# Kernel tuning notes

Measured on AMD Instinct MI355X. Metric: run time of the kernel, lower is better.

The kernel has to match this reference:

```python
import jax, jax.numpy as jnp
import numpy as np

# GraphConvolutionSparse forward:
#   x = sparse_dropout(X)            (dropout=0.0 -> identity, kept faithful)
#   h = X @ W                        (sparse-dense matmul via segment_sum)
#   h = A @ h                        (sparse-dense matmul via segment_sum)
#   out = relu(h)

DROPOUT = 0.0  # layer default; keep_prob = 1 - dropout

def setup_inputs() -> dict:
    key = jax.random.key(0)
    k1, k2, k3, k4, k5, k6, k7 = jax.random.split(key, 7)
    N = 100000       # nodes
    D_IN = 512       # input feature dim
    D_OUT = 128      # output feature dim
    NNZ_X = 800000   # nonzeros in sparse feature matrix
    N_E = 1600000    # adjacency nonzeros (edges)
    x_vals = jax.random.normal(k1, (NNZ_X,), dtype=jnp.float32)
    x_rows = jax.random.randint(k2, (NNZ_X,), 0, N, dtype=jnp.int32)
    x_cols = jax.random.randint(k3, (NNZ_X,), 0, D_IN, dtype=jnp.int32)
    adj_vals = jax.random.uniform(k4, (N_E,), dtype=jnp.float32)
    adj_rows = jax.random.randint(k5, (N_E,), 0, N, dtype=jnp.int32)
    adj_cols = jax.random.randint(k6, (N_E,), 0, N, dtype=jnp.int32)
    init_range = np.sqrt(6.0 / (D_IN + D_OUT)).astype(np.float32)
    W = jax.random.uniform(k7, (D_IN, D_OUT), minval=-init_range, maxval=init_range, dtype=jnp.float32)
    return {"x_vals": x_vals, "x_rows": x_rows, "x_cols": x_cols,
            "adj_vals": adj_vals, "adj_rows": adj_rows, "adj_cols": adj_cols,
            "W": W, "n_nodes": N}

def reference(x_vals, x_rows, x_cols, adj_vals, adj_rows, adj_cols, W, n_nodes):
    keep_prob = 1.0 - DROPOUT
    # sparse dropout: with dropout=0.0 the mask keeps all entries and scale is 1,
    # so it reduces to the deterministic identity (faithful to tf semantics).
    vals = x_vals * (1.0 / keep_prob)
    # h = X @ W : gather weight rows by feature column, scale, scatter-add by node row
    xw = jax.ops.segment_sum(vals[:, None] * W[x_cols], x_rows, num_segments=n_nodes)  # [N, D_OUT]
    # out = A @ h : gather source-node rows, scale by edge weight, scatter-add to dest
    agg = jax.ops.segment_sum(adj_vals[:, None] * xw[adj_cols], adj_rows, num_segments=n_nodes)  # [N, D_OUT]
    return jax.nn.relu(agg)
```

## Files before the change

### kernel.cpp

```cpp
#include <hip/hip_runtime.h>
#include <hip/hip_fp16.h>


#define DOUT 128
#define RBB 128
#define RBB_BITS 7
#define NKEY 128
#define NBIN 1024
#define NBMAX 4096
#define COLMASK 131071
#define CTH 512
#define NW 8
#define CAPX 1536
#define CAPA 3072
#define SCB 4096

static inline size_t align_up(size_t x, size_t a) { return (x + a - 1) & ~(a - 1); }

__device__ inline int2 nt_load_int2(const int2* p) {
    long long v = __builtin_nontemporal_load((const long long*)p);
    int2 r; r.x = (int)(unsigned int)(v & 0xffffffffLL); r.y = (int)(v >> 32);
    return r;
}
__device__ inline void nt_store_float2(float2* p, float2 v) {
    union { float2 f; long long l; } u; u.f = v;
    __builtin_nontemporal_store(u.l, (long long*)p);
}

__device__ inline int wave_incl_scan(int v, int lane) {
    #pragma unroll
    for (int off = 1; off < 64; off <<= 1) {
        int up = __shfl_up(v, off, 64);
        if (lane >= off) v += up;
    }
    return v;
}

__global__ __launch_bounds__(256) void prep_kernel(int* __restrict__ cnts, int ncnt,
                                                   const float* __restrict__ W,
                                                   __half2* __restrict__ Wh, int whtot) {
    int i = blockIdx.x * 256 + threadIdx.x;
    if (i < ncnt) cnts[i] = 0;
    if (i < whtot) {
        int c = i >> 6, l = i & 63;
        Wh[i] = __floats2half2_rn(W[(c << 7) + 2 * l], W[(c << 7) + 2 * l + 1]);
    }
}

__global__ __launch_bounds__(256) void hist_coarse(const int* __restrict__ xr, int nx,
                                                   const int* __restrict__ ar, int na,
                                                   int* __restrict__ cx, int* __restrict__ ca) {
    __shared__ int h[2 * NBMAX];
    for (int i = threadIdx.x; i < 2 * NBMAX; i += 256) h[i] = 0;
    __syncthreads();
    int base = blockIdx.x * 4096;
    int tot = nx + na;
    #pragma unroll
    for (int k = 0; k < 16; ++k) {
        int i = base + k * 256 + threadIdx.x;
        if (i < tot) {
            if (i < nx) atomicAdd(&h[xr[i] >> RBB_BITS], 1);
            else        atomicAdd(&h[NBMAX + (ar[i - nx] >> RBB_BITS)], 1);
        }
    }
    __syncthreads();
    for (int i = threadIdx.x; i < 2 * NBMAX; i += 256) {
        int c = h[i];
        if (c) {
            if (i < NBMAX) atomicAdd(&cx[i], c);
            else           atomicAdd(&ca[i - NBMAX], c);
        }
    }
}

__global__ __launch_bounds__(1024) void scan_nb(const int* __restrict__ cx, const int* __restrict__ ca,
                                                int* __restrict__ bx, int* __restrict__ ba,
                                                int* __restrict__ curx, int* __restrict__ cura, int nb) {
    const int* c = blockIdx.x ? ca : cx;
    int* bs  = blockIdx.x ? ba : bx;
    int* cur = blockIdx.x ? cura : curx;
    __shared__ int wsum[16];
    __shared__ int woff[16];
    __shared__ int carry_s, chunk_tot;
    int tid = threadIdx.x, lane = tid & 63, wid = tid >> 6;
    if (tid == 0) carry_s = 0;
    __syncthreads();
    for (int base = 0; base < nb; base += 1024) {
        int i = base + tid;
        int v = (i < nb) ? c[i] : 0;
        int incl = wave_incl_scan(v, lane);
        if (lane == 63) wsum[wid] = incl;
        __syncthreads();
        if (wid == 0 && lane < 16) {
            int s = wsum[lane];
            int is = s;
            #pragma unroll
            for (int off = 1; off < 16; off <<= 1) {
                int up = __shfl_up(is, off, 64);
                if (lane >= off) is += up;
            }
            woff[lane] = is - s;
            if (lane == 15) chunk_tot = is;
        }
        __syncthreads();
        int excl = incl - v + woff[wid] + carry_s;
        if (i < nb) { bs[i] = excl; cur[i] = excl; }
        __syncthreads();
        if (tid == 0) carry_s += chunk_tot;
        __syncthreads();
    }
    if (tid == 0) bs[nb] = carry_s;
}

__global__ __launch_bounds__(512) void bucket_scatter2(const int* __restrict__ xr, const int* __restrict__ xc,
                                                       const float* __restrict__ xv, int nx,
                                                       const int* __restrict__ ar, const int* __restrict__ ac,
                                                       const float* __restrict__ av, int na,
                                                       int* __restrict__ curx, int* __restrict__ cura,
                                                       int2* __restrict__ stx, int2* __restrict__ sta,
                                                       int nb, int nblk_x, int capx, int capa) {
    const int* rows; const int* cols; const float* vals; int n;
    int* gcur; int2* stage; int base; int cap;
    if (blockIdx.x < nblk_x) {
        rows = xr; cols = xc; vals = xv; n = nx; gcur = curx; stage = stx;
        base = blockIdx.x * SCB; cap = capx;
    } else {
        rows = ar; cols = ac; vals = av; n = na; gcur = cura; stage = sta;
        base = (blockIdx.x - nblk_x) * SCB; cap = capa;
    }
    __shared__ int2 sp[SCB];
    __shared__ unsigned short bin16[SCB];
    __shared__ int cnt[NBIN];
    __shared__ int lbase[NBIN];
    __shared__ int gb[NBIN];
    __shared__ int tot_s;
    int tid = threadIdx.x, lane = tid & 63, wid = tid >> 6;
    for (int i = tid; i < NBIN; i += 512) cnt[i] = 0;
    __syncthreads();
    int rr[8]; int cc[8]; float vv[8];
    #pragma unroll
    for (int k = 0; k < 8; ++k) {
        int i = base + k * 512 + tid;
        rr[k] = -1;
        if (i < n) {
            rr[k] = __builtin_nontemporal_load(&rows[i]);
            cc[k] = __builtin_nontemporal_load(&cols[i]);
            vv[k] = __builtin_nontemporal_load(&vals[i]);
            atomicAdd(&cnt[rr[k] >> RBB_BITS], 1);
        }
    }
    __syncthreads();
    if (wid == 0) {
        int carry = 0;
        #pragma unroll
        for (int q = 0; q < NBIN / 64; ++q) {
            int k = (q << 6) + lane;
            int v = cnt[k];
            int incl = wave_incl_scan(v, lane) + carry;
            lbase[k] = incl - v;
            carry = __shfl(incl, 63, 64);
        }
        if (lane == 0) tot_s = carry;
    }
    __syncthreads();
    for (int b = tid; b < nb; b += 512) {
        int c = cnt[b];
        if (c) gb[b] = atomicAdd(&gcur[b], c);
        cnt[b] = lbase[b];
    }
    __syncthreads();
    #pragma unroll
    for (int k = 0; k < 8; ++k) {
        if (rr[k] >= 0) {
            int b = rr[k] >> RBB_BITS;
            int p = atomicAdd(&cnt[b], 1);
            sp[p] = make_int2(((rr[k] & (RBB - 1)) << 17) | cc[k], __float_as_int(vv[k]));
            bin16[p] = (unsigned short)b;
        }
    }
    __syncthreads();
    int tot = tot_s;
    for (int p = tid; p < tot; p += 512) {
        int2 e = sp[p];
        int b = bin16[p];
        int q = p - lbase[b];
        int r = gb[b];
        if (cap > 0) {
            int slot = r + q;
            if (slot < cap) stage[b * cap + slot] = e;
        } else {
            stage[r + q] = e;
        }
    }
}


__global__ __launch_bounds__(CTH) void consumer_xw(const int* __restrict__ bx, const int* __restrict__ gcnt,
                                                   const int2* __restrict__ stage,
                                                   const __half2* __restrict__ Wh, __half2* __restrict__ xwh,
                                                   int N, int cap) {
    __shared__ int2 sp[CAPX];
    __shared__ int hoff[NKEY + 1];
    __shared__ int curs[NKEY];
    int b = blockIdx.x;
    int s, cnt;
    if (cap > 0) { s = b * cap; cnt = min(gcnt[b], cap); }
    else         { s = bx[b]; cnt = bx[b + 1] - s; }
    int tid = threadIdx.x, lane = tid & 63, wid = tid >> 6;
    bool fast = (cnt <= CAPX);
    if (tid < NKEY) curs[tid] = 0;
    __syncthreads();
    int2 pr[3];
    if (fast) {
        #pragma unroll
        for (int k = 0; k < 3; ++k) {
            int i = k * CTH + tid;
            if (i < cnt) {
                pr[k] = nt_load_int2(&stage[s + i]);
                atomicAdd(&curs[(pr[k].x >> 17) & (NKEY - 1)], 1);
            }
        }
    }
    __syncthreads();
    if (wid == 0) {
        int carry = 0;
        #pragma unroll
        for (int q = 0; q < 2; ++q) {
            int k = (q << 6) + lane;
            int v = curs[k];
            int incl = wave_incl_scan(v, lane) + carry;
            hoff[k] = incl - v;
            curs[k] = incl - v;
            carry = __shfl(incl, 63, 64);
        }
        if (lane == 0) hoff[NKEY] = carry;
    }
    __syncthreads();
    if (fast) {
        #pragma unroll
        for (int k = 0; k < 3; ++k) {
            int i = k * CTH + tid;
            if (i < cnt) {
                int r = (pr[k].x >> 17) & (NKEY - 1);
                sp[atomicAdd(&curs[r], 1)] = pr[k];
            }
        }
    }
    __syncthreads();
    int row0 = b << RBB_BITS;
    #pragma unroll 1
    for (int rr = 0; rr < NKEY / NW; ++rr) {
        int r = wid + rr * NW;
        int grow = row0 + r;
        if (grow >= N) continue;
        float ax = 0.f, ay = 0.f;
        if (fast) {
            int j = hoff[r], o1 = hoff[r + 1];
            for (; j + 3 < o1; j += 4) {
                int2 c0 = sp[j], c1 = sp[j + 1], c2 = sp[j + 2], c3 = sp[j + 3];
                float2 w0 = __half22float2(Wh[((size_t)(c0.x & COLMASK) << 6) + lane]);
                float2 w1 = __half22float2(Wh[((size_t)(c1.x & COLMASK) << 6) + lane]);
                float2 w2 = __half22float2(Wh[((size_t)(c2.x & COLMASK) << 6) + lane]);
                float2 w3 = __half22float2(Wh[((size_t)(c3.x & COLMASK) << 6) + lane]);
                float v0 = __int_as_float(c0.y), v1 = __int_as_float(c1.y);
                float v2 = __int_as_float(c2.y), v3 = __int_as_float(c3.y);
                ax += v0 * w0.x + v1 * w1.x + v2 * w2.x + v3 * w3.x;
                ay += v0 * w0.y + v1 * w1.y + v2 * w2.y + v3 * w3.y;
            }
            for (; j < o1; ++j) {
                int2 c0 = sp[j];
                float2 w0 = __half22float2(Wh[((size_t)(c0.x & COLMASK) << 6) + lane]);
                float v0 = __int_as_float(c0.y);
                ax += v0 * w0.x; ay += v0 * w0.y;
            }
        } else {
            for (int j = 0; j < cnt; ++j) {
                int2 c0 = stage[s + j];
                if (((c0.x >> 17) & (NKEY - 1)) == r) {
                    float2 w0 = __half22float2(Wh[((size_t)(c0.x & COLMASK) << 6) + lane]);
                    float v0 = __int_as_float(c0.y);
                    ax += v0 * w0.x; ay += v0 * w0.y;
                }
            }
        }
        xwh[((size_t)grow << 6) + lane] = __float22half2_rn(make_float2(ax, ay));
    }
}

__global__ __launch_bounds__(CTH) void consumer_adj(const int* __restrict__ ba, const int* __restrict__ gcnt,
                                                    const int2* __restrict__ stage,
                                                    const __half2* __restrict__ xwh, float* __restrict__ out,
                                                    int N, int cap) {
    __shared__ int2 sp[CAPA];
    __shared__ int hoff[NKEY + 1];
    __shared__ int curs[NKEY];
    int b = blockIdx.x;
    int s, cnt;
    if (cap > 0) { s = b * cap; cnt = min(gcnt[b], cap); }
    else         { s = ba[b]; cnt = ba[b + 1] - s; }
    int tid = threadIdx.x, lane = tid & 63, wid = tid >> 6;
    bool fast = (cnt <= CAPA);
    if (tid < NKEY) curs[tid] = 0;
    __syncthreads();
    int2 pr[6];
    if (fast) {
        #pragma unroll
        for (int k = 0; k < 6; ++k) {
            int i = k * CTH + tid;
            if (i < cnt) {
                pr[k] = nt_load_int2(&stage[s + i]);
                atomicAdd(&curs[(pr[k].x >> 17) & (NKEY - 1)], 1);
            }
        }
    }
    __syncthreads();
    if (wid == 0) {
        int carry = 0;
        #pragma unroll
        for (int q = 0; q < 2; ++q) {
            int k = (q << 6) + lane;
            int v = curs[k];
            int incl = wave_incl_scan(v, lane) + carry;
            hoff[k] = incl - v;
            curs[k] = incl - v;
            carry = __shfl(incl, 63, 64);
        }
        if (lane == 0) hoff[NKEY] = carry;
    }
    __syncthreads();
    if (fast) {
        #pragma unroll
        for (int k = 0; k < 6; ++k) {
            int i = k * CTH + tid;
            if (i < cnt) {
                int r = (pr[k].x >> 17) & (NKEY - 1);
                sp[atomicAdd(&curs[r], 1)] = pr[k];
            }
        }
    }
    __syncthreads();
    int row0 = b << RBB_BITS;
    #pragma unroll 1
    for (int rr = 0; rr < NKEY / NW; ++rr) {
        int r = wid + rr * NW;
        int grow = row0 + r;
        if (grow >= N) continue;
        float ax = 0.f, ay = 0.f;
        if (fast) {
            int j = hoff[r], o1 = hoff[r + 1];
            for (; j + 3 < o1; j += 4) {
                int2 c0 = sp[j], c1 = sp[j + 1], c2 = sp[j + 2], c3 = sp[j + 3];
                float2 h0 = __half22float2(xwh[((size_t)(c0.x & COLMASK) << 6) + lane]);
                float2 h1 = __half22float2(xwh[((size_t)(c1.x & COLMASK) << 6) + lane]);
                float2 h2 = __half22float2(xwh[((size_t)(c2.x & COLMASK) << 6) + lane]);
                float2 h3 = __half22float2(xwh[((size_t)(c3.x & COLMASK) << 6) + lane]);
                float v0 = __int_as_float(c0.y), v1 = __int_as_float(c1.y);
                float v2 = __int_as_float(c2.y), v3 = __int_as_float(c3.y);
                ax += v0 * h0.x + v1 * h1.x + v2 * h2.x + v3 * h3.x;
                ay += v0 * h0.y + v1 * h1.y + v2 * h2.y + v3 * h3.y;
            }
            for (; j < o1; ++j) {
                int2 c0 = sp[j];
                float2 h0 = __half22float2(xwh[((size_t)(c0.x & COLMASK) << 6) + lane]);
                float v0 = __int_as_float(c0.y);
                ax += v0 * h0.x; ay += v0 * h0.y;
            }
        } else {
            for (int j = 0; j < cnt; ++j) {
                int2 c0 = stage[s + j];
                if (((c0.x >> 17) & (NKEY - 1)) == r) {
                    float2 h0 = __half22float2(xwh[((size_t)(c0.x & COLMASK) << 6) + lane]);
                    float v0 = __int_as_float(c0.y);
                    ax += v0 * h0.x; ay += v0 * h0.y;
                }
            }
        }
        nt_store_float2(&((float2*)(out + (size_t)grow * DOUT))[lane],
                        make_float2(fmaxf(ax, 0.f), fmaxf(ay, 0.f)));
    }
}

__global__ void spmm_xw_atomic(const float* __restrict__ x_vals, const int* __restrict__ x_rows,
                               const int* __restrict__ x_cols, const float* __restrict__ W,
                               float* __restrict__ xw, int nnz) {
    long long t = (long long)blockIdx.x * blockDim.x + threadIdx.x;
    int i = (int)(t >> 7), d = (int)(t & 127);
    if (i >= nnz) return;
    atomicAdd(&xw[(long long)x_rows[i] * DOUT + d], x_vals[i] * W[(long long)x_cols[i] * DOUT + d]);
}
__global__ void spmm_adj_atomic(const float* __restrict__ adj_vals, const int* __restrict__ adj_rows,
                                const int* __restrict__ adj_cols, const float* __restrict__ xw,
                                float* __restrict__ out, int n_e) {
    long long t = (long long)blockIdx.x * blockDim.x + threadIdx.x;
    int e = (int)(t >> 7), d = (int)(t & 127);
    if (e >= n_e) return;
    atomicAdd(&out[(long long)adj_rows[e] * DOUT + d], adj_vals[e] * xw[(long long)adj_cols[e] * DOUT + d]);
}
__global__ void relu_kernel(float4* __restrict__ out, int n4) {
    int i = blockIdx.x * blockDim.x + threadIdx.x;
    if (i >= n4) return;
    float4 v = out[i];
    v.x = fmaxf(v.x, 0.f); v.y = fmaxf(v.y, 0.f);
    v.z = fmaxf(v.z, 0.f); v.w = fmaxf(v.w, 0.f);
    out[i] = v;
}

extern "C" void kernel_launch(void* const* d_in, const int* in_sizes, int n_in,
                              void* d_out, int out_size, void* d_ws, size_t ws_size,
                              hipStream_t stream) {
    const float* x_vals   = (const float*)d_in[0];
    const int*   x_rows   = (const int*)d_in[1];
    const int*   x_cols   = (const int*)d_in[2];
    const float* adj_vals = (const float*)d_in[3];
    const int*   adj_rows = (const int*)d_in[4];
    const int*   adj_cols = (const int*)d_in[5];
    const float* W        = (const float*)d_in[6];
    float* out = (float*)d_out;

    const int nnz_x = in_sizes[0];
    const int n_e   = in_sizes[3];
    const int N     = out_size / DOUT;
    const int D_IN  = in_sizes[6] / DOUT;
    const int nbc   = (N + RBB - 1) / RBB;

    char* ws = (char*)d_ws;
    size_t off = 0;
    size_t xw_off   = off; off = align_up(off + (size_t)N * DOUT * sizeof(__half), 128);
    size_t wh_off   = off; off = align_up(off + (size_t)D_IN * 64 * sizeof(__half2), 128);
    size_t cx_off   = off; off += (size_t)NBMAX * sizeof(int);
    size_t ca_off   = off; off = align_up(off + (size_t)NBMAX * sizeof(int), 128);
    size_t bx_off   = off; off = align_up(off + (size_t)(NBMAX + 1) * sizeof(int), 128);
    size_t baoff    = off; off = align_up(off + (size_t)(NBMAX + 1) * sizeof(int), 128);
    size_t head = off;
    size_t sxc_off = head;
    size_t sac_off = align_up(sxc_off + (size_t)nbc * CAPX * sizeof(int2), 128);
    size_t needed_cap = align_up(sac_off + (size_t)nbc * CAPA * sizeof(int2), 128);
    size_t sxm_off = head;
    size_t sam_off = align_up(sxm_off + (size_t)nnz_x * sizeof(int2), 128);
    size_t needed_mid = align_up(sam_off + (size_t)n_e * sizeof(int2), 128);

    bool ok_dims = (nbc <= NBIN) && (N <= (COLMASK + 1));
    const int ncnt = 2 * NBMAX;
    const int whtot = D_IN * 64;
    const int prep_n = (ncnt > whtot ? ncnt : whtot);

    if (ok_dims && ws_size >= needed_cap) {
        __half2* xwh  = (__half2*)(ws + xw_off);
        __half2* Wh   = (__half2*)(ws + wh_off);
        int*  cx      = (int*)(ws + cx_off);
        int*  ca      = (int*)(ws + ca_off);
        int2* stage_x = (int2*)(ws + sxc_off);
        int2* stage_a = (int2*)(ws + sac_off);

        prep_kernel<<<(prep_n + 255) / 256, 256, 0, stream>>>(cx, ncnt, W, Wh, whtot);

        int nblk_x = (nnz_x + SCB - 1) / SCB;
        int nblk_a = (n_e + SCB - 1) / SCB;
        bucket_scatter2<<<nblk_x + nblk_a, 512, 0, stream>>>(x_rows, x_cols, x_vals, nnz_x,
                                                             adj_rows, adj_cols, adj_vals, n_e,
                                                             cx, ca, stage_x, stage_a,
                                                             nbc, nblk_x, CAPX, CAPA);
        consumer_xw<<<nbc, CTH, 0, stream>>>(nullptr, cx, stage_x, Wh, xwh, N, CAPX);
        consumer_adj<<<nbc, CTH, 0, stream>>>(nullptr, ca, stage_a, xwh, out, N, CAPA);
    } else if (ok_dims && ws_size >= needed_mid) {
        __half2* xwh  = (__half2*)(ws + xw_off);
        __half2* Wh   = (__half2*)(ws + wh_off);
        int*  cx      = (int*)(ws + cx_off);
        int*  ca      = (int*)(ws + ca_off);
        int*  bx      = (int*)(ws + bx_off);
        int*  ba      = (int*)(ws + baoff);
        int2* stage_x = (int2*)(ws + sxm_off);
        int2* stage_a = (int2*)(ws + sam_off);

        prep_kernel<<<(prep_n + 255) / 256, 256, 0, stream>>>(cx, ncnt, W, Wh, whtot);

        int tot = nnz_x + n_e;
        hist_coarse<<<(tot + 4095) / 4096, 256, 0, stream>>>(x_rows, nnz_x, adj_rows, n_e, cx, ca);
        scan_nb<<<2, 1024, 0, stream>>>(cx, ca, bx, ba, cx, ca, nbc);

        int nblk_x = (nnz_x + SCB - 1) / SCB;
        int nblk_a = (n_e + SCB - 1) / SCB;
        bucket_scatter2<<<nblk_x + nblk_a, 512, 0, stream>>>(x_rows, x_cols, x_vals, nnz_x,
                                                             adj_rows, adj_cols, adj_vals, n_e,
                                                             cx, ca, stage_x, stage_a,
                                                             nbc, nblk_x, 0, 0);
        consumer_xw<<<nbc, CTH, 0, stream>>>(bx, nullptr, stage_x, Wh, xwh, N, 0);
        consumer_adj<<<nbc, CTH, 0, stream>>>(ba, nullptr, stage_a, xwh, out, N, 0);
    } else {
        float* xw = (float*)ws;
        hipMemsetAsync(xw, 0, (size_t)out_size * sizeof(float), stream);
        hipMemsetAsync(out, 0, (size_t)out_size * sizeof(float), stream);
        long long t1 = (long long)nnz_x * DOUT;
        spmm_xw_atomic<<<(int)((t1 + 255) / 256), 256, 0, stream>>>(x_vals, x_rows, x_cols, W, xw, nnz_x);
        long long t2 = (long long)n_e * DOUT;
        spmm_adj_atomic<<<(int)((t2 + 255) / 256), 256, 0, stream>>>(adj_vals, adj_rows, adj_cols, xw, out, n_e);
        relu_kernel<<<(out_size / 4 + 255) / 256, 256, 0, stream>>>((float4*)out, out_size / 4);
    }
}
```

Baseline: 201.6 us.

## Fuse adjacency bucket scatter with X@W consumer in one launch

Splits the combined scatter launch so the first kernel buckets only the X entries. The adjacency scatter then runs in the same grid as the X@W consumer blocks, letting the two independent phases overlap and removing one kernel launch boundary. The fused kernel reserves a larger shared buffer (the scatter size) for every block, so the consumer blocks may run at lower occupancy.

```diff
diff --git a/kernel.cpp b/kernel.cpp
--- a/kernel.cpp
+++ b/kernel.cpp
@@ -112,28 +112,17 @@
     if (tid == 0) bs[nb] = carry_s;
 }
 
-__global__ __launch_bounds__(512) void bucket_scatter2(const int* __restrict__ xr, const int* __restrict__ xc,
-                                                       const float* __restrict__ xv, int nx,
-                                                       const int* __restrict__ ar, const int* __restrict__ ac,
-                                                       const float* __restrict__ av, int na,
-                                                       int* __restrict__ curx, int* __restrict__ cura,
-                                                       int2* __restrict__ stx, int2* __restrict__ sta,
-                                                       int nb, int nblk_x, int capx, int capa) {
-    const int* rows; const int* cols; const float* vals; int n;
-    int* gcur; int2* stage; int base; int cap;
-    if (blockIdx.x < nblk_x) {
-        rows = xr; cols = xc; vals = xv; n = nx; gcur = curx; stage = stx;
-        base = blockIdx.x * SCB; cap = capx;
-    } else {
-        rows = ar; cols = ac; vals = av; n = na; gcur = cura; stage = sta;
-        base = (blockIdx.x - nblk_x) * SCB; cap = capa;
-    }
-    __shared__ int2 sp[SCB];
-    __shared__ unsigned short bin16[SCB];
-    __shared__ int cnt[NBIN];
-    __shared__ int lbase[NBIN];
-    __shared__ int gb[NBIN];
-    __shared__ int tot_s;
+__device__ inline void scatter_body(char* smem,
+                                    const int* __restrict__ rows, const int* __restrict__ cols,
+                                    const float* __restrict__ vals, int n, int base,
+                                    int* __restrict__ gcur, int2* __restrict__ stage,
+                                    int nb, int cap) {
+    int2* sp            = (int2*)smem;
+    unsigned short* b16 = (unsigned short*)(smem + 32768);
+    int* cnt            = (int*)(smem + 40960);
+    int* lbase          = (int*)(smem + 45056);
+    int* gb             = (int*)(smem + 49152);
+    int* tot_s          = (int*)(smem + 53248);
     int tid = threadIdx.x, lane = tid & 63, wid = tid >> 6;
     for (int i = tid; i < NBIN; i += 512) cnt[i] = 0;
     __syncthreads();
@@ -160,7 +149,7 @@
             lbase[k] = incl - v;
             carry = __shfl(incl, 63, 64);
         }
-        if (lane == 0) tot_s = carry;
+        if (lane == 0) tot_s[0] = carry;
     }
     __syncthreads();
     for (int b = tid; b < nb; b += 512) {
@@ -175,14 +164,14 @@
             int b = rr[k] >> RBB_BITS;
             int p = atomicAdd(&cnt[b], 1);
             sp[p] = make_int2(((rr[k] & (RBB - 1)) << 17) | cc[k], __float_as_int(vv[k]));
-            bin16[p] = (unsigned short)b;
-        }
-    }
-    __syncthreads();
-    int tot = tot_s;
+            b16[p] = (unsigned short)b;
+        }
+    }
+    __syncthreads();
+    int tot = tot_s[0];
     for (int p = tid; p < tot; p += 512) {
         int2 e = sp[p];
-        int b = bin16[p];
+        int b = b16[p];
         int q = p - lbase[b];
         int r = gb[b];
         if (cap > 0) {
@@ -194,15 +183,14 @@
     }
 }
 
-
-__global__ __launch_bounds__(CTH) void consumer_xw(const int* __restrict__ bx, const int* __restrict__ gcnt,
-                                                   const int2* __restrict__ stage,
-                                                   const __half2* __restrict__ Wh, __half2* __restrict__ xwh,
-                                                   int N, int cap) {
-    __shared__ int2 sp[CAPX];
-    __shared__ int hoff[NKEY + 1];
-    __shared__ int curs[NKEY];
-    int b = blockIdx.x;
+__device__ inline void xw_body(char* smem, int b,
+                               const int* __restrict__ bx, const int* __restrict__ gcnt,
+                               const int2* __restrict__ stage,
+                               const __half2* __restrict__ Wh, __half2* __restrict__ xwh,
+                               int N, int cap) {
+    int2* sp  = (int2*)smem;
+    int* hoff = (int*)(smem + 12288);
+    int* curs = (int*)(smem + 12804);
     int s, cnt;
     if (cap > 0) { s = b * cap; cnt = min(gcnt[b], cap); }
     else         { s = bx[b]; cnt = bx[b + 1] - s; }
@@ -287,6 +275,46 @@
     }
 }
 
+__global__ __launch_bounds__(512) void bucket_scatter2(const int* __restrict__ xr, const int* __restrict__ xc,
+                                                       const float* __restrict__ xv, int nx,
+                                                       const int* __restrict__ ar, const int* __restrict__ ac,
+                                                       const float* __restrict__ av, int na,
+                                                       int* __restrict__ curx, int* __restrict__ cura,
+                                                       int2* __restrict__ stx, int2* __restrict__ sta,
+                                                       int nb, int nblk_x, int capx, int capa) {
+    __shared__ char smem[53252] __attribute__((aligned(16)));
+    if (blockIdx.x < nblk_x) {
+        scatter_body(smem, xr, xc, xv, nx, blockIdx.x * SCB, curx, stx, nb, capx);
+    } else {
+        scatter_body(smem, ar, ac, av, na, (blockIdx.x - nblk_x) * SCB, cura, sta, nb, capa);
+    }
+}
+
+__global__ __launch_bounds__(512) void scatter_a_xw(const int* __restrict__ ar, const int* __restrict__ ac,
+                                                    const float* __restrict__ av, int na,
+                                                    int* __restrict__ cura, int2* __restrict__ sta,
+                                                    int nblk_a, int capa,
+                                                    const int* __restrict__ gcntx, const int2* __restrict__ stage_x,
+                                                    const __half2* __restrict__ Wh, __half2* __restrict__ xwh,
+                                                    int N, int capx, int nb) {
+    __shared__ char smem[53252] __attribute__((aligned(16)));
+    if (blockIdx.x < nblk_a) {
+        scatter_body(smem, ar, ac, av, na, blockIdx.x * SCB, cura, sta, nb, capa);
+    } else {
+        int b = blockIdx.x - nblk_a;
+        xw_body(smem, b, nullptr, gcntx, stage_x, Wh, xwh, N, capx);
+    }
+}
+
+__global__ __launch_bounds__(CTH) void consumer_xw(const int* __restrict__ bx, const int* __restrict__ gcnt,
+                                                   const int2* __restrict__ stage,
+                                                   const __half2* __restrict__ Wh, __half2* __restrict__ xwh,
+                                                   int N, int cap) {
+    __shared__ char smem[13316] __attribute__((aligned(16)));
+    xw_body(smem, blockIdx.x, bx, gcnt, stage, Wh, xwh, N, cap);
+}
+
+
 __global__ __launch_bounds__(CTH) void consumer_adj(const int* __restrict__ ba, const int* __restrict__ gcnt,
                                                     const int2* __restrict__ stage,
                                                     const __half2* __restrict__ xwh, float* __restrict__ out,
@@ -456,11 +484,13 @@
 
         int nblk_x = (nnz_x + SCB - 1) / SCB;
         int nblk_a = (n_e + SCB - 1) / SCB;
-        bucket_scatter2<<<nblk_x + nblk_a, 512, 0, stream>>>(x_rows, x_cols, x_vals, nnz_x,
-                                                             adj_rows, adj_cols, adj_vals, n_e,
-                                                             cx, ca, stage_x, stage_a,
-                                                             nbc, nblk_x, CAPX, CAPA);
-        consumer_xw<<<nbc, CTH, 0, stream>>>(nullptr, cx, stage_x, Wh, xwh, N, CAPX);
+        bucket_scatter2<<<nblk_x, 512, 0, stream>>>(x_rows, x_cols, x_vals, nnz_x,
+                                                    adj_rows, adj_cols, adj_vals, n_e,
+                                                    cx, ca, stage_x, stage_a,
+                                                    nbc, nblk_x, CAPX, CAPA);
+        scatter_a_xw<<<nblk_a + nbc, 512, 0, stream>>>(adj_rows, adj_cols, adj_vals, n_e,
+                                                       ca, stage_a, nblk_a, CAPA,
+                                                       cx, stage_x, Wh, xwh, N, CAPX, nbc);
         consumer_adj<<<nbc, CTH, 0, stream>>>(nullptr, ca, stage_a, xwh, out, N, CAPA);
     } else if (ok_dims && ws_size >= needed_mid) {
         __half2* xwh  = (__half2*)(ws + xw_off);
```

Result: slower. 213.0 us (+5.7%).

## Cache fp16 weight matrix in LDS with persistent grid for X@W consumer

Applied to the files above, without the earlier changes.

Adds a persistent consumer_xw variant in which each block loads the whole fp16 W (512x128, 128 KB) into shared memory once, then loops over row buckets with a grid-stride loop capped at 256 blocks. Weight gathers then hit LDS instead of global/L2 memory. In exchange each block uses about 128 KB+ of LDS, so occupancy drops to one block per CU, and the copy of W is paid per block. The MI355X's 160 KB LDS per CU is what makes this possible.

```diff
diff --git a/kernel.cpp b/kernel.cpp
--- a/kernel.cpp
+++ b/kernel.cpp
@@ -14,6 +14,7 @@
 #define CAPX 1536
 #define CAPA 3072
 #define SCB 4096
+#define WHL4MAX 8192
 
 static inline size_t align_up(size_t x, size_t a) { return (x + a - 1) & ~(a - 1); }
 
@@ -194,6 +195,104 @@
     }
 }
 
+
+__global__ __launch_bounds__(CTH) void consumer_xw_lds(const int* __restrict__ gcnt,
+                                                       const int2* __restrict__ stage,
+                                                       const __half2* __restrict__ Wh,
+                                                       __half2* __restrict__ xwh,
+                                                       int N, int cap, int nbc, int whint4) {
+    __shared__ int4 WhL4[WHL4MAX];
+    __shared__ int2 sp[CAPX];
+    __shared__ int hoff[NKEY + 1];
+    __shared__ int curs[NKEY];
+    int tid = threadIdx.x, lane = tid & 63, wid = tid >> 6;
+    const int4* Wh4 = (const int4*)Wh;
+    for (int i = tid; i < whint4; i += CTH) WhL4[i] = Wh4[i];
+    const __half2* WhL = (const __half2*)WhL4;
+    for (int b = blockIdx.x; b < nbc; b += gridDim.x) {
+        int s = b * cap;
+        int cnt = min(gcnt[b], cap);
+        bool fast = (cnt <= CAPX);
+        if (tid < NKEY) curs[tid] = 0;
+        __syncthreads();
+        int2 pr[3];
+        if (fast) {
+            #pragma unroll
+            for (int k = 0; k < 3; ++k) {
+                int i = k * CTH + tid;
+                if (i < cnt) {
+                    pr[k] = nt_load_int2(&stage[s + i]);
+                    atomicAdd(&curs[(pr[k].x >> 17) & (NKEY - 1)], 1);
+                }
+            }
+        }
+        __syncthreads();
+        if (wid == 0) {
+            int carry = 0;
+            #pragma unroll
+            for (int q = 0; q < 2; ++q) {
+                int k = (q << 6) + lane;
+                int v = curs[k];
+                int incl = wave_incl_scan(v, lane) + carry;
+                hoff[k] = incl - v;
+                curs[k] = incl - v;
+                carry = __shfl(incl, 63, 64);
+            }
+            if (lane == 0) hoff[NKEY] = carry;
+        }
+        __syncthreads();
+        if (fast) {
+            #pragma unroll
+            for (int k = 0; k < 3; ++k) {
+                int i = k * CTH + tid;
+                if (i < cnt) {
+                    int r = (pr[k].x >> 17) & (NKEY - 1);
+                    sp[atomicAdd(&curs[r], 1)] = pr[k];
+                }
+            }
+        }
+        __syncthreads();
+        int row0 = b << RBB_BITS;
+        #pragma unroll 1
+        for (int rr = 0; rr < NKEY / NW; ++rr) {
+            int r = wid + rr * NW;
+            int grow = row0 + r;
+            if (grow >= N) continue;
+            float ax = 0.f, ay = 0.f;
+            if (fast) {
+                int j = hoff[r], o1 = hoff[r + 1];
+                for (; j + 3 < o1; j += 4) {
+                    int2 c0 = sp[j], c1 = sp[j + 1], c2 = sp[j + 2], c3 = sp[j + 3];
+                    float2 w0 = __half22float2(WhL[((c0.x & COLMASK) << 6) + lane]);
+                    float2 w1 = __half22float2(WhL[((c1.x & COLMASK) << 6) + lane]);
+                    float2 w2 = __half22float2(WhL[((c2.x & COLMASK) << 6) + lane]);
+                    float2 w3 = __half22float2(WhL[((c3.x & COLMASK) << 6) + lane]);
+                    float v0 = __int_as_float(c0.y), v1 = __int_as_float(c1.y);
+                    float v2 = __int_as_float(c2.y), v3 = __int_as_float(c3.y);
+                    ax += v0 * w0.x + v1 * w1.x + v2 * w2.x + v3 * w3.x;
+                    ay += v0 * w0.y + v1 * w1.y + v2 * w2.y + v3 * w3.y;
+                }
+                for (; j < o1; ++j) {
+                    int2 c0 = sp[j];
+                    float2 w0 = __half22float2(WhL[((c0.x & COLMASK) << 6) + lane]);
+                    float v0 = __int_as_float(c0.y);
+                    ax += v0 * w0.x; ay += v0 * w0.y;
+                }
+            } else {
+                for (int j = 0; j < cnt; ++j) {
+                    int2 c0 = stage[s + j];
+                    if (((c0.x >> 17) & (NKEY - 1)) == r) {
+                        float2 w0 = __half22float2(WhL[((c0.x & COLMASK) << 6) + lane]);
+                        float v0 = __int_as_float(c0.y);
+                        ax += v0 * w0.x; ay += v0 * w0.y;
+                    }
+                }
+            }
+            xwh[((size_t)grow << 6) + lane] = __float22half2_rn(make_float2(ax, ay));
+        }
+        __syncthreads();
+    }
+}
 
 __global__ __launch_bounds__(CTH) void consumer_xw(const int* __restrict__ bx, const int* __restrict__ gcnt,
                                                    const int2* __restrict__ stage,
@@ -287,6 +386,7 @@
     }
 }
 
+
 __global__ __launch_bounds__(CTH) void consumer_adj(const int* __restrict__ ba, const int* __restrict__ gcnt,
                                                     const int2* __restrict__ stage,
                                                     const __half2* __restrict__ xwh, float* __restrict__ out,
@@ -460,7 +560,12 @@
                                                              adj_rows, adj_cols, adj_vals, n_e,
                                                              cx, ca, stage_x, stage_a,
                                                              nbc, nblk_x, CAPX, CAPA);
-        consumer_xw<<<nbc, CTH, 0, stream>>>(nullptr, cx, stage_x, Wh, xwh, N, CAPX);
+        if (D_IN <= 512) {
+            int gxw = (nbc < 256) ? nbc : 256;
+            consumer_xw_lds<<<gxw, CTH, 0, stream>>>(cx, stage_x, Wh, xwh, N, CAPX, nbc, D_IN * 16);
+        } else {
+            consumer_xw<<<nbc, CTH, 0, stream>>>(nullptr, cx, stage_x, Wh, xwh, N, CAPX);
+        }
         consumer_adj<<<nbc, CTH, 0, stream>>>(nullptr, ca, stage_a, xwh, out, N, CAPA);
     } else if (ok_dims && ws_size >= needed_mid) {
         __half2* xwh  = (__half2*)(ws + xw_off);
```

Measured after the change: 219.0 us. 1.09x slower.
